# Kernel optimization log

Measured on AMD Instinct MI355X. Metric: run time of the kernel, lower is better.

The kernel has to match this reference:

```python
import jax, jax.numpy as jnp
import numpy as np

EPS_LOG = 2.220446049250313e-16  # np.finfo(float).eps used in ES_EE.ee
K = 2  # use_experts (top-k)


def _balance(v):
    v = v.astype(jnp.float32)
    # torch .var() is unbiased (ddof=1)
    return jnp.var(v, ddof=1) / (jnp.mean(v) ** 2 + 1e-10)


def setup_inputs() -> dict:
    key = jax.random.key(0)
    ks = jax.random.split(key, 8)
    B, C, H, W, E, D, HF = 2, 128, 128, 128, 6, 6, 512
    s = 0.02  # small init so exp(expert_out) stays in range
    return {
        "x": jax.random.normal(ks[0], (B, C, H, W), jnp.float32),
        "prompt": jax.random.normal(ks[1], (B, C), jnp.float32),
        "de_cls": jax.random.uniform(ks[2], (B, D), jnp.float32),
        "w_g": jax.random.normal(ks[3], (2 * C, E), jnp.float32) * s,
        "gate_boost": jnp.asarray(0.5, jnp.float32),
        "degra_w": jax.random.normal(ks[4], (D, E), jnp.float32) * s,
        "degra_b": jnp.zeros((E,), jnp.float32),
        "fc1_w": jax.random.normal(ks[5], (E, C, HF), jnp.float32) * s,
        "fc1_b": jnp.zeros((E, HF), jnp.float32),
        "fc2_w": jax.random.normal(ks[6], (E, HF, C), jnp.float32) * s,
        "fc2_b": jnp.zeros((E, C), jnp.float32),
    }


def reference(x, prompt, de_cls, w_g, gate_boost, degra_w, degra_b,
              fc1_w, fc1_b, fc2_w, fc2_b):
    # eval-mode forward (self.training == False -> no gating noise)
    B, C, H, W = x.shape
    N = B * H * W
    xf = jnp.transpose(x, (0, 2, 3, 1)).reshape(N, C)           # (b h w) c
    pf = jnp.broadcast_to(prompt[:, None, None, :], (B, H, W, C)).reshape(N, C)
    D = de_cls.shape[1]
    df = jnp.broadcast_to(de_cls[:, None, None, :], (B, H, W, D)).reshape(N, D)

    x_p = jnp.concatenate([xf, pf], axis=1)                     # [N, 2C]
    expert_bias = df @ degra_w + degra_b                        # degra_proj
    logits = x_p @ w_g + gate_boost * expert_bias               # [N, E]

    top_v, top_i = jax.lax.top_k(logits, K)
    gates_k = jax.nn.softmax(top_v, axis=1)                     # [N, K]
    w = jnp.zeros_like(logits).at[jnp.arange(N)[:, None], top_i].set(gates_k)

    Weight = w.sum(0)                                           # [E]
    s_load = (w > 0).sum(0).astype(jnp.float32)                 # w_load
    loss = _balance(Weight) + _balance(s_load)

    # per-expert Mlp on all tokens (w==0 rows contribute nothing to combine,
    # mathematically identical to the gather/scatter dispatch in ES_EE)
    hid = jax.nn.gelu(jnp.einsum('nc,ech->neh', xf, fc1_w) + fc1_b,
                      approximate=False)                        # [N, E, HF]
    out = jnp.einsum('neh,ehc->nec', hid, fc2_w) + fc2_b        # [N, E, C]

    # ES_EE.ee: log( sum_e gate_e * exp(out_e) ), zeros -> eps
    comb = jnp.einsum('ne,nec->nc', w, jnp.exp(out))
    comb = jnp.where(comb == 0, EPS_LOG, comb)
    y = jnp.log(comb)

    y = y.reshape(B, H, W, C).transpose(0, 3, 1, 2)             # b c h w
    return y, loss
```

## Files before the change

### kernel.cpp

```cpp
#include <hip/hip_runtime.h>
#include <math.h>

#define HW    16384
#define NTOK  32768
#define CDIM  128
#define HFDIM 512
#define NEXP  6

typedef __attribute__((ext_vector_type(8))) short short8;
typedef __attribute__((ext_vector_type(8))) unsigned short ushort8v;
typedef __attribute__((ext_vector_type(16))) float f32x16;
typedef unsigned long long u64;

#define OFF_XFB    0UL
#define OFF_LIST   8388608UL
#define OFF_GATES  9175040UL
#define OFF_OUTBUF 9437184UL
#define OFF_WT1    42991616UL
#define OFF_WT2    43778048UL
#define OFF_BIAS   44564480UL
#define OFF_CNT    44564736UL
#define OFF_WSUM   44564992UL

__device__ __forceinline__ unsigned int bf16_1(float f) {
    unsigned int u = __float_as_uint(f);
    return (u + 0x7FFFu + ((u >> 16) & 1)) >> 16;
}
__device__ __forceinline__ unsigned int bf16pair(float lo, float hi) {
    return bf16_1(lo) | (bf16_1(hi) << 16);
}
__device__ __forceinline__ float gelu_f(float v) {
    return __fdividef(v, 1.0f + __expf(-1.702f * v));
}
__device__ __forceinline__ short8 mk8(unsigned a, unsigned b, unsigned c, unsigned d) {
    union { unsigned u[4]; short8 s; } x;
    x.u[0] = a; x.u[1] = b; x.u[2] = c; x.u[3] = d;
    return x.s;
}

#define GLDS16(src, dst) __builtin_amdgcn_global_load_lds( \
    (const __attribute__((address_space(1))) void*)(src),  \
    (__attribute__((address_space(3))) void*)(dst), 16, 0, 0)

__device__ __forceinline__ f32x16 MFMA_B(short8 a, short8 b, f32x16 c) {
    return __builtin_amdgcn_mfma_f32_32x32x16_bf16(a, b, c, 0, 0, 0);
}

__global__ __launch_bounds__(64) void prep_kernel(
    const float* __restrict__ prompt, const float* __restrict__ de_cls,
    const float* __restrict__ w_g, const float* __restrict__ gate_boost,
    const float* __restrict__ degra_w, const float* __restrict__ degra_b,
    float* __restrict__ bias, int* __restrict__ cnt, float* __restrict__ wsum)
{
    int t = threadIdx.x;
    if (t < 2 * NEXP) {
        int b = t / NEXP, e = t % NEXP;
        float acc = 0.f;
        for (int c = 0; c < CDIM; ++c)
            acc = fmaf(prompt[b*CDIM + c], w_g[(CDIM + c)*NEXP + e], acc);
        float db = 0.f;
        for (int d = 0; d < 6; ++d)
            db = fmaf(de_cls[b*6 + d], degra_w[d*NEXP + e], db);
        bias[b*NEXP + e] = acc + gate_boost[0] * (db + degra_b[e]);
    }
    if (t >= 32 && t < 32 + NEXP) cnt[t - 32] = 0;
    if (t >= 40 && t < 40 + NEXP) wsum[t - 40] = 0.f;
}

__global__ __launch_bounds__(256) void wconv_kernel(
    const float* __restrict__ fc1_w, const float* __restrict__ fc2_w,
    unsigned short* __restrict__ wt1, unsigned short* __restrict__ wt2)
{
    __shared__ unsigned short ls[128][128];
    const int bid = blockIdx.x;
    const int e = bid >> 3, which = (bid >> 2) & 1, ch = bid & 3;
    const int t = threadIdx.x;
    #pragma unroll 4
    for (int i = 0; i < 16; ++i) {
        int id = t + 256 * i;
        int k = id >> 5, q = id & 31;
        const float* p = which
            ? (fc2_w + (size_t)e*65536 + (size_t)(ch*128 + k)*128 + q*4)
            : (fc1_w + (size_t)e*65536 + (size_t)k*512 + ch*128 + q*4);
        float4 v = *(const float4*)p;
        u64 pk = (u64)bf16_1(v.x) | ((u64)bf16_1(v.y) << 16)
               | ((u64)bf16_1(v.z) << 32) | ((u64)bf16_1(v.w) << 48);
        *(u64*)&ls[k][q*4] = pk;
    }
    __syncthreads();
    unsigned short* dst = (which ? wt2 : wt1) + (((size_t)(e*4 + ch)) << 14);
    #pragma unroll 2
    for (int i = 0; i < 8; ++i) {
        int id = t + 256 * i;
        int col = id & 127, kg = id >> 7;
        unsigned short v[8];
        #pragma unroll
        for (int j = 0; j < 8; ++j) v[j] = ls[kg*8 + j][col];
        int4 pk;
        pk.x = v[0] | (v[1] << 16); pk.y = v[2] | (v[3] << 16);
        pk.z = v[4] | (v[5] << 16); pk.w = v[6] | (v[7] << 16);
        *(int4*)(dst + (size_t)col*128 + (((kg ^ (col & 15)) & 15) << 3)) = pk;
    }
}

__global__ __launch_bounds__(256) void gate_kernel(
    const float* __restrict__ x, const float* __restrict__ w_g,
    const float* __restrict__ bias, unsigned short* __restrict__ xfb,
    int* __restrict__ list, float* __restrict__ gates,
    int* __restrict__ cnt, float* __restrict__ wsum)
{
    __shared__ float xs[CDIM][65];
    __shared__ float wgs[CDIM][NEXP];
    __shared__ int   cnt_s[NEXP];
    __shared__ float ws_s[NEXP];
    __shared__ int   base_s[NEXP];
    const int t = threadIdx.x;
    const int n0 = blockIdx.x * 64;
    const int b = n0 >> 14;
    const int hw0 = n0 & (HW - 1);

    for (int i = t; i < CDIM * NEXP; i += 256) wgs[i / NEXP][i % NEXP] = w_g[i];
    if (t < NEXP) { cnt_s[t] = 0; ws_s[t] = 0.f; }

    const float* xb = x + (size_t)b * CDIM * HW + hw0;
    #pragma unroll 4
    for (int i = 0; i < 32; ++i) {
        int idx = t + 256 * i;
        int c = idx >> 6, j = idx & 63;
        xs[c][j] = xb[(size_t)c * HW + j];
    }
    __syncthreads();
    unsigned int* xo = (unsigned int*)xfb;
    #pragma unroll 4
    for (int i = 0; i < 16; ++i) {
        int idx = t + 256 * i;
        int tk = idx >> 6, cp = idx & 63;
        xo[(size_t)(n0 + tk) * 64 + cp] = bf16pair(xs[2*cp][tk], xs[2*cp+1][tk]);
    }

    int i0 = 0, i1 = 0, s0 = 0, s1 = 0;
    float g0 = 0.f, g1 = 0.f;
    if (t < 64) {
        float lg[NEXP];
        #pragma unroll
        for (int e = 0; e < NEXP; ++e) lg[e] = bias[b*NEXP + e];
        for (int c = 0; c < CDIM; ++c) {
            float xv = xs[c][t];
            #pragma unroll
            for (int e = 0; e < NEXP; ++e) lg[e] = fmaf(xv, wgs[c][e], lg[e]);
        }
        i0 = 0;
        #pragma unroll
        for (int e = 1; e < NEXP; ++e) if (lg[e] > lg[i0]) i0 = e;
        i1 = (i0 == 0) ? 1 : 0;
        #pragma unroll
        for (int e = 0; e < NEXP; ++e) if (e != i0 && lg[e] > lg[i1]) i1 = e;
        float e1 = expf(lg[i1] - lg[i0]);
        g0 = 1.f / (1.f + e1);
        g1 = e1 * g0;
        s0 = atomicAdd(&cnt_s[i0], 1);
        s1 = atomicAdd(&cnt_s[i1], 1);
        atomicAdd(&ws_s[i0], g0);
        atomicAdd(&ws_s[i1], g1);
    }
    __syncthreads();
    if (t < NEXP) {
        base_s[t] = atomicAdd(&cnt[t], cnt_s[t]);
        atomicAdd(&wsum[t], ws_s[t]);
    }
    __syncthreads();
    if (t < 64) {
        int n = n0 + t;
        list[i0 * NTOK + base_s[i0] + s0] = 2 * n;
        list[i1 * NTOK + base_s[i1] + s1] = 2 * n + 1;
        gates[2 * n]     = g0;
        gates[2 * n + 1] = g1;
    }
}

__global__ void loss_kernel(const int* __restrict__ cnt,
                            const float* __restrict__ wsum,
                            float* __restrict__ out_loss)
{
    if (threadIdx.x == 0 && blockIdx.x == 0) {
        float mw = 0.f, mc = 0.f;
        for (int e = 0; e < NEXP; ++e) { mw += wsum[e]; mc += (float)cnt[e]; }
        mw /= NEXP; mc /= NEXP;
        float vw = 0.f, vc = 0.f;
        for (int e = 0; e < NEXP; ++e) {
            float dw = wsum[e] - mw, dc = (float)cnt[e] - mc;
            vw += dw * dw; vc += dc * dc;
        }
        vw /= (NEXP - 1); vc /= (NEXP - 1);
        out_loss[0] = vw / (mw * mw + 1e-10f) + vc / (mc * mc + 1e-10f);
    }
}

__global__ __launch_bounds__(256, 2) void expert_kernel(
    const unsigned short* __restrict__ xfb, const int* __restrict__ list,
    const int* __restrict__ cnt, const float* __restrict__ gates,
    const unsigned short* __restrict__ wt1, const unsigned short* __restrict__ wt2,
    const float* __restrict__ fc1_b, const float* __restrict__ fc2_b,
    unsigned short* __restrict__ outbuf)
{
    __shared__ unsigned short w1c[16384];
    __shared__ unsigned short w2c[16384];
    const int e = blockIdx.x;
    const int ne = cnt[e];
    const int base = blockIdx.y * 128;
    if (base >= ne) return;
    const int t = threadIdx.x;
    const int w = t >> 6, l = t & 63;
    const int l31 = l & 31, lk = (l >> 5) * 8;
    const bool islo = (l < 32);

    int r = base + w*32 + l31;
    int a = (r < ne) ? list[e*NTOK + r] : -1;
    float g = (a >= 0) ? gates[a] : 0.f;
    int tok = (a >= 0) ? (a >> 1) : 0;

    short8 afr[8];
    {
        const unsigned short* xr = xfb + (size_t)tok*128 + lk;
        #pragma unroll
        for (int ks = 0; ks < 8; ++ks)
            afr[ks] = *(const short8*)(xr + ks*16);
    }

    f32x16 zz;
    #pragma unroll
    for (int i = 0; i < 16; ++i) zz[i] = 0.0f;
    f32x16 oacc[4] = {zz, zz, zz, zz};

    for (int gp = 0; gp < 4; ++gp) {
        {
            const unsigned short* s1 = wt1 + (((size_t)(e*4 + gp)) << 14) + w*4096 + l*8;
            const unsigned short* s2 = wt2 + (((size_t)(e*4 + gp)) << 14) + w*4096 + l*8;
            #pragma unroll
            for (int i = 0; i < 8; ++i)
                GLDS16(s1 + i*512, &w1c[w*4096 + i*512]);
            #pragma unroll
            for (int i = 0; i < 8; ++i)
                GLDS16(s2 + i*512, &w2c[w*4096 + i*512]);
        }
        __syncthreads();

        short8 pa[8];
        #pragma unroll
        for (int ch = 0; ch < 4; ++ch) {
            f32x16 c1 = zz;
            int arow = ch*32 + l31;
            #pragma unroll
            for (int ks = 0; ks < 8; ++ks) {
                int k = ks*16 + lk;
                short8 wf = *(const short8*)((const char*)w1c + arow*256
                             + ((((k >> 3) ^ (arow & 15)) & 15) << 4));
                c1 = MFMA_B(wf, afr[ks], c1);
            }
            const float* bb = fc1_b + (size_t)e*HFDIM + gp*128 + ch*32 + 4*(l >> 5);
            float4 b0 = *(const float4*)(bb);
            float4 b1 = *(const float4*)(bb + 8);
            float4 b2 = *(const float4*)(bb + 16);
            float4 b3 = *(const float4*)(bb + 24);
            float bias[16] = {b0.x, b0.y, b0.z, b0.w, b1.x, b1.y, b1.z, b1.w,
                              b2.x, b2.y, b2.z, b2.w, b3.x, b3.y, b3.z, b3.w};
            unsigned int pr[8];
            #pragma unroll
            for (int i = 0; i < 8; ++i) {
                float h0 = gelu_f(c1[2*i]     + bias[2*i]);
                float h1 = gelu_f(c1[2*i + 1] + bias[2*i + 1]);
                pr[i] = bf16pair(h0, h1);
            }
            unsigned int rx0 = __shfl_xor(islo ? pr[2] : pr[0], 32);
            unsigned int rx1 = __shfl_xor(islo ? pr[3] : pr[1], 32);
            unsigned int rx2 = __shfl_xor(islo ? pr[6] : pr[4], 32);
            unsigned int rx3 = __shfl_xor(islo ? pr[7] : pr[5], 32);
            pa[2*ch]     = mk8(islo ? pr[0] : rx0, islo ? pr[1] : rx1,
                               islo ? rx0 : pr[2], islo ? rx1 : pr[3]);
            pa[2*ch + 1] = mk8(islo ? pr[4] : rx2, islo ? pr[5] : rx3,
                               islo ? rx2 : pr[6], islo ? rx3 : pr[7]);
        }
        #pragma unroll
        for (int kg = 0; kg < 8; ++kg) {
            #pragma unroll
            for (int ct = 0; ct < 4; ++ct) {
                int crow = ct*32 + l31;
                short8 bf = *(const short8*)((const char*)w2c + crow*256
                             + ((((kg*2 + (l >> 5)) ^ (crow & 15)) & 15) << 4));
                oacc[ct] = MFMA_B(pa[kg], bf, oacc[ct]);
            }
        }
        __syncthreads();
    }

    float bc[4];
    #pragma unroll
    for (int ct = 0; ct < 4; ++ct)
        bc[ct] = fc2_b[(size_t)e*CDIM + ct*32 + l31];
    #pragma unroll
    for (int rr = 0; rr < 16; ++rr) {
        int crow = (rr & 3) + 8*(rr >> 2) + 4*(l >> 5);
        int av   = __shfl(a, crow);
        float gv = __shfl(g, crow);
        if (av < 0) continue;
        unsigned short* po = outbuf + (size_t)av*CDIM + l31;
        #pragma unroll
        for (int ct = 0; ct < 4; ++ct)
            po[ct*32] = (unsigned short)bf16_1(gv * __expf(oacc[ct][rr] + bc[ct]));
    }
}

__global__ __launch_bounds__(256) void combine_kernel(
    const unsigned short* __restrict__ outbuf, float* __restrict__ out)
{
    __shared__ float ys[64][129];
    const int t = threadIdx.x;
    const int n0 = blockIdx.x * 64;
    const int b = n0 >> 14;
    const int hw0 = n0 & (HW - 1);
    #pragma unroll
    for (int i = 0; i < 4; ++i) {
        int idx = t + 256 * i;
        int tk = idx >> 4, c8 = (idx & 15) * 8;
        const unsigned short* p = outbuf + (size_t)(n0 + tk) * 256 + c8;
        ushort8v p0 = *(const ushort8v*)p;
        ushort8v p1 = *(const ushort8v*)(p + 128);
        const float EPSL = 2.2204460492503131e-16f;
        #pragma unroll
        for (int j = 0; j < 8; ++j) {
            float v = __uint_as_float((unsigned)p0[j] << 16)
                    + __uint_as_float((unsigned)p1[j] << 16);
            ys[tk][c8 + j] = __logf(v == 0.f ? EPSL : v);
        }
    }
    __syncthreads();
    float* ob = out + (size_t)b * CDIM * HW + hw0;
    #pragma unroll 4
    for (int i = 0; i < 32; ++i) {
        int idx = t + 256 * i;
        int c = idx >> 6;
        int j = idx & 63;
        ob[(size_t)c * HW + j] = ys[j][c];
    }
}

extern "C" void kernel_launch(void* const* d_in, const int* in_sizes, int n_in,
                              void* d_out, int out_size, void* d_ws, size_t ws_size,
                              hipStream_t stream)
{
    const float* x       = (const float*)d_in[0];
    const float* prompt  = (const float*)d_in[1];
    const float* de_cls  = (const float*)d_in[2];
    const float* w_g     = (const float*)d_in[3];
    const float* gboost  = (const float*)d_in[4];
    const float* degra_w = (const float*)d_in[5];
    const float* degra_b = (const float*)d_in[6];
    const float* fc1_w   = (const float*)d_in[7];
    const float* fc1_b   = (const float*)d_in[8];
    const float* fc2_w   = (const float*)d_in[9];
    const float* fc2_b   = (const float*)d_in[10];
    float* out = (float*)d_out;
    char* ws = (char*)d_ws;

    unsigned short* xfb  = (unsigned short*)(ws + OFF_XFB);
    int*   list   = (int*)(ws + OFF_LIST);
    float* gates  = (float*)(ws + OFF_GATES);
    unsigned short* outbuf = (unsigned short*)(ws + OFF_OUTBUF);
    unsigned short* wt1 = (unsigned short*)(ws + OFF_WT1);
    unsigned short* wt2 = (unsigned short*)(ws + OFF_WT2);
    float* bias   = (float*)(ws + OFF_BIAS);
    int*   cnt    = (int*)(ws + OFF_CNT);
    float* wsum   = (float*)(ws + OFF_WSUM);

    prep_kernel<<<1, 64, 0, stream>>>(prompt, de_cls, w_g, gboost, degra_w,
                                      degra_b, bias, cnt, wsum);
    wconv_kernel<<<48, 256, 0, stream>>>(fc1_w, fc2_w, wt1, wt2);
    gate_kernel<<<512, 256, 0, stream>>>(x, w_g, bias, xfb, list, gates, cnt, wsum);
    loss_kernel<<<1, 64, 0, stream>>>(cnt, wsum, out + (size_t)NTOK * CDIM);
    dim3 eg(NEXP, 256);
    expert_kernel<<<eg, 256, 0, stream>>>(xfb, list, cnt, gates, wt1, wt2,
                                          fc1_b, fc2_b, outbuf);
    combine_kernel<<<512, 256, 0, stream>>>(outbuf, out);
}
```

Measured before the change: 125.1 us.

## Shrink expert blocks to 64 tokens and split output channels into halves

The expert kernel now runs 128-thread blocks over 64 tokens each, with twice as many blocks in the grid. Each block makes two passes, one per half of the 128 output channels. Weight tiles in shared memory are halved, and each thread keeps only two output accumulators instead of four. The aim is to cut register and LDS pressure so more waves fit per CU. The cost is that the first GEMM (fc1 plus GELU) is recomputed in each pass, so that work doubles, and there are more barriers and weight loads.

After: 181.2 us. 44.9% more time.

```diff
diff --git a/kernel.cpp b/kernel.cpp
--- a/kernel.cpp
+++ b/kernel.cpp
@@ -196,22 +196,22 @@
     }
 }
 
-__global__ __launch_bounds__(256, 2) void expert_kernel(
+__global__ __launch_bounds__(128, 4) void expert_kernel(
     const unsigned short* __restrict__ xfb, const int* __restrict__ list,
     const int* __restrict__ cnt, const float* __restrict__ gates,
     const unsigned short* __restrict__ wt1, const unsigned short* __restrict__ wt2,
     const float* __restrict__ fc1_b, const float* __restrict__ fc2_b,
     unsigned short* __restrict__ outbuf)
 {
-    __shared__ unsigned short w1c[16384];
-    __shared__ unsigned short w2c[16384];
+    __shared__ unsigned short w1c[8192];
+    __shared__ unsigned short w2c[8192];
     const int e = blockIdx.x;
     const int ne = cnt[e];
-    const int base = blockIdx.y * 128;
+    const int base = blockIdx.y * 64;
     if (base >= ne) return;
     const int t = threadIdx.x;
     const int w = t >> 6, l = t & 63;
-    const int l31 = l & 31, lk = (l >> 5) * 8;
+    const int l31 = l & 31, lh = l >> 5;
     const bool islo = (l < 32);
 
     int r = base + w*32 + l31;
@@ -221,7 +221,7 @@
 
     short8 afr[8];
     {
-        const unsigned short* xr = xfb + (size_t)tok*128 + lk;
+        const unsigned short* xr = xfb + (size_t)tok*128 + lh*8;
         #pragma unroll
         for (int ks = 0; ks < 8; ++ks)
             afr[ks] = *(const short8*)(xr + ks*16);
@@ -230,83 +230,88 @@
     f32x16 zz;
     #pragma unroll
     for (int i = 0; i < 16; ++i) zz[i] = 0.0f;
-    f32x16 oacc[4] = {zz, zz, zz, zz};
-
-    for (int gp = 0; gp < 4; ++gp) {
-        {
-            const unsigned short* s1 = wt1 + (((size_t)(e*4 + gp)) << 14) + w*4096 + l*8;
-            const unsigned short* s2 = wt2 + (((size_t)(e*4 + gp)) << 14) + w*4096 + l*8;
+
+    for (int p = 0; p < 2; ++p) {
+        f32x16 oacc0 = zz, oacc1 = zz;
+        for (int gp = 0; gp < 8; ++gp) {
+            {
+                const unsigned short* s1 = wt1 + (((size_t)(e*4 + (gp >> 1))) << 14)
+                                         + (gp & 1)*8192 + w*4096 + l*8;
+                #pragma unroll
+                for (int i = 0; i < 8; ++i)
+                    GLDS16(s1 + i*512, &w1c[w*4096 + i*512]);
+                if ((gp & 1) == 0) {
+                    const unsigned short* s2 = wt2 + (((size_t)(e*4 + (gp >> 1))) << 14)
+                                             + p*8192 + w*4096 + l*8;
+                    #pragma unroll
+                    for (int i = 0; i < 8; ++i)
+                        GLDS16(s2 + i*512, &w2c[w*4096 + i*512]);
+                }
+            }
+            __syncthreads();
+
             #pragma unroll
-            for (int i = 0; i < 8; ++i)
-                GLDS16(s1 + i*512, &w1c[w*4096 + i*512]);
-            #pragma unroll
-            for (int i = 0; i < 8; ++i)
-                GLDS16(s2 + i*512, &w2c[w*4096 + i*512]);
-        }
-        __syncthreads();
-
-        short8 pa[8];
-        #pragma unroll
-        for (int ch = 0; ch < 4; ++ch) {
-            f32x16 c1 = zz;
-            int arow = ch*32 + l31;
-            #pragma unroll
-            for (int ks = 0; ks < 8; ++ks) {
-                int k = ks*16 + lk;
-                short8 wf = *(const short8*)((const char*)w1c + arow*256
-                             + ((((k >> 3) ^ (arow & 15)) & 15) << 4));
-                c1 = MFMA_B(wf, afr[ks], c1);
+            for (int ch = 0; ch < 2; ++ch) {
+                f32x16 c1 = zz;
+                int arow = ch*32 + l31;
+                #pragma unroll
+                for (int ks = 0; ks < 8; ++ks) {
+                    int kk = ks*2 + lh;
+                    short8 wf = *(const short8*)((const char*)w1c + arow*256
+                                 + (((kk ^ (arow & 15)) & 15) << 4));
+                    c1 = MFMA_B(wf, afr[ks], c1);
+                }
+                const float* bb = fc1_b + (size_t)e*HFDIM + gp*64 + ch*32 + 4*lh;
+                float4 b0 = *(const float4*)(bb);
+                float4 b1 = *(const float4*)(bb + 8);
+                float4 b2 = *(const float4*)(bb + 16);
+                float4 b3 = *(const float4*)(bb + 24);
+                float bias[16] = {b0.x, b0.y, b0.z, b0.w, b1.x, b1.y, b1.z, b1.w,
+                                  b2.x, b2.y, b2.z, b2.w, b3.x, b3.y, b3.z, b3.w};
+                unsigned int pr[8];
+                #pragma unroll
+                for (int i = 0; i < 8; ++i) {
+                    float h0 = gelu_f(c1[2*i]     + bias[2*i]);
+                    float h1 = gelu_f(c1[2*i + 1] + bias[2*i + 1]);
+                    pr[i] = bf16pair(h0, h1);
+                }
+                unsigned int rx0 = __shfl_xor(islo ? pr[2] : pr[0], 32);
+                unsigned int rx1 = __shfl_xor(islo ? pr[3] : pr[1], 32);
+                unsigned int rx2 = __shfl_xor(islo ? pr[6] : pr[4], 32);
+                unsigned int rx3 = __shfl_xor(islo ? pr[7] : pr[5], 32);
+                short8 pa0 = mk8(islo ? pr[0] : rx0, islo ? pr[1] : rx1,
+                                 islo ? rx0 : pr[2], islo ? rx1 : pr[3]);
+                short8 pa1 = mk8(islo ? pr[4] : rx2, islo ? pr[5] : rx3,
+                                 islo ? rx2 : pr[6], islo ? rx3 : pr[7]);
+                int kg0 = (gp & 1)*4 + ch*2;
+                #pragma unroll
+                for (int ct = 0; ct < 2; ++ct) {
+                    int crow = ct*32 + l31;
+                    const char* cb = (const char*)w2c + crow*256;
+                    short8 bf0 = *(const short8*)(cb
+                                 + ((((kg0*2 + lh) ^ (crow & 15)) & 15) << 4));
+                    short8 bf1 = *(const short8*)(cb
+                                 + (((((kg0 + 1)*2 + lh) ^ (crow & 15)) & 15) << 4));
+                    if (ct == 0) { oacc0 = MFMA_B(pa0, bf0, oacc0);
+                                   oacc0 = MFMA_B(pa1, bf1, oacc0); }
+                    else         { oacc1 = MFMA_B(pa0, bf0, oacc1);
+                                   oacc1 = MFMA_B(pa1, bf1, oacc1); }
+                }
             }
-            const float* bb = fc1_b + (size_t)e*HFDIM + gp*128 + ch*32 + 4*(l >> 5);
-            float4 b0 = *(const float4*)(bb);
-            float4 b1 = *(const float4*)(bb + 8);
-            float4 b2 = *(const float4*)(bb + 16);
-            float4 b3 = *(const float4*)(bb + 24);
-            float bias[16] = {b0.x, b0.y, b0.z, b0.w, b1.x, b1.y, b1.z, b1.w,
-                              b2.x, b2.y, b2.z, b2.w, b3.x, b3.y, b3.z, b3.w};
-            unsigned int pr[8];
-            #pragma unroll
-            for (int i = 0; i < 8; ++i) {
-                float h0 = gelu_f(c1[2*i]     + bias[2*i]);
-                float h1 = gelu_f(c1[2*i + 1] + bias[2*i + 1]);
-                pr[i] = bf16pair(h0, h1);
-            }
-            unsigned int rx0 = __shfl_xor(islo ? pr[2] : pr[0], 32);
-            unsigned int rx1 = __shfl_xor(islo ? pr[3] : pr[1], 32);
-            unsigned int rx2 = __shfl_xor(islo ? pr[6] : pr[4], 32);
-            unsigned int rx3 = __shfl_xor(islo ? pr[7] : pr[5], 32);
-            pa[2*ch]     = mk8(islo ? pr[0] : rx0, islo ? pr[1] : rx1,
-                               islo ? rx0 : pr[2], islo ? rx1 : pr[3]);
-            pa[2*ch + 1] = mk8(islo ? pr[4] : rx2, islo ? pr[5] : rx3,
-                               islo ? rx2 : pr[6], islo ? rx3 : pr[7]);
-        }
-        #pragma unroll
-        for (int kg = 0; kg < 8; ++kg) {
-            #pragma unroll
-            for (int ct = 0; ct < 4; ++ct) {
-                int crow = ct*32 + l31;
-                short8 bf = *(const short8*)((const char*)w2c + crow*256
-                             + ((((kg*2 + (l >> 5)) ^ (crow & 15)) & 15) << 4));
-                oacc[ct] = MFMA_B(pa[kg], bf, oacc[ct]);
-            }
-        }
-        __syncthreads();
-    }
-
-    float bc[4];
-    #pragma unroll
-    for (int ct = 0; ct < 4; ++ct)
-        bc[ct] = fc2_b[(size_t)e*CDIM + ct*32 + l31];
-    #pragma unroll
-    for (int rr = 0; rr < 16; ++rr) {
-        int crow = (rr & 3) + 8*(rr >> 2) + 4*(l >> 5);
-        int av   = __shfl(a, crow);
-        float gv = __shfl(g, crow);
-        if (av < 0) continue;
-        unsigned short* po = outbuf + (size_t)av*CDIM + l31;
-        #pragma unroll
-        for (int ct = 0; ct < 4; ++ct)
-            po[ct*32] = (unsigned short)bf16_1(gv * __expf(oacc[ct][rr] + bc[ct]));
+            __syncthreads();
+        }
+        float bc0 = fc2_b[(size_t)e*CDIM + p*64 + l31];
+        float bc1 = fc2_b[(size_t)e*CDIM + p*64 + 32 + l31];
+        #pragma unroll
+        for (int rr = 0; rr < 16; ++rr) {
+            int crow = (rr & 3) + 8*(rr >> 2) + 4*lh;
+            int av   = __shfl(a, crow);
+            float gv = __shfl(g, crow);
+            if (av < 0) continue;
+            unsigned short* po = outbuf + (size_t)av*CDIM + p*64 + l31;
+            po[0]  = (unsigned short)bf16_1(gv * __expf(oacc0[rr] + bc0));
+            po[32] = (unsigned short)bf16_1(gv * __expf(oacc1[rr] + bc1));
+        }
     }
 }
 
@@ -377,8 +382,8 @@
     wconv_kernel<<<48, 256, 0, stream>>>(fc1_w, fc2_w, wt1, wt2);
     gate_kernel<<<512, 256, 0, stream>>>(x, w_g, bias, xfb, list, gates, cnt, wsum);
     loss_kernel<<<1, 64, 0, stream>>>(cnt, wsum, out + (size_t)NTOK * CDIM);
-    dim3 eg(NEXP, 256);
-    expert_kernel<<<eg, 256, 0, stream>>>(xfb, list, cnt, gates, wt1, wt2,
+    dim3 eg(NEXP, 512);
+    expert_kernel<<<eg, 128, 0, stream>>>(xfb, list, cnt, gates, wt1, wt2,
                                           fc1_b, fc2_b, outbuf);
     combine_kernel<<<512, 256, 0, stream>>>(outbuf, out);
 }
```
